# Kernel tuning notes

Measured on AMD Instinct MI355X. Metric: run time of the kernel, lower is better.

## Reference

```python
import jax, jax.numpy as jnp
import numpy as np

NEG_SLOPE = 0.2  # PyG GATConv default LeakyReLU slope
EPS = 1e-16
LN_EPS = 1e-5


def setup_inputs() -> dict:
    key = jax.random.key(0)
    ks = jax.random.split(key, 12)
    N, E, HID, H = 10000, 320000, 256, 4
    C = HID // H
    s = 1.0 / np.sqrt(HID)
    x = jax.random.normal(ks[0], (N, HID), jnp.float32)
    src = jax.random.randint(ks[1], (E,), 0, N, dtype=jnp.int32)
    dst = jax.random.randint(ks[2], (E,), 0, N, dtype=jnp.int32)
    edge_index = jnp.stack([src, dst])
    edge_attr = jax.random.normal(ks[3], (E, 1), jnp.float32)
    W = jax.random.normal(ks[4], (HID, HID), jnp.float32) * s
    att_src = jax.random.normal(ks[5], (H, C), jnp.float32) * s
    att_dst = jax.random.normal(ks[6], (H, C), jnp.float32) * s
    We = jax.random.normal(ks[7], (1, HID), jnp.float32) * s
    att_edge = jax.random.normal(ks[8], (H, C), jnp.float32) * s
    bias = jnp.zeros((HID,), jnp.float32)
    gamma = jnp.ones((HID,), jnp.float32)
    beta = jnp.zeros((HID,), jnp.float32)
    return {"x": x, "edge_index": edge_index, "edge_attr": edge_attr, "W": W,
            "att_src": att_src, "att_dst": att_dst, "We": We,
            "att_edge": att_edge, "bias": bias, "gamma": gamma, "beta": beta}


def _gat_layer(x, edge_index, edge_attr, W, att_src, att_dst, We, att_edge,
               bias, gamma, beta):
    N, HID = x.shape
    H, C = att_src.shape
    src, dst = edge_index[0], edge_index[1]

    # add_self_loops=True with fill_value='mean': self-loop edge_attr is the
    # mean of incoming edge features per node (0 if no incoming edges).
    ones = jnp.ones((src.shape[0],), x.dtype)
    deg = jax.ops.segment_sum(ones, dst, num_segments=N)
    loop_attr = jax.ops.segment_sum(edge_attr, dst, num_segments=N) \
        / jnp.maximum(deg, 1.0)[:, None]
    loop_idx = jnp.arange(N, dtype=src.dtype)
    src = jnp.concatenate([src, loop_idx])
    dst = jnp.concatenate([dst, loop_idx])
    e_attr = jnp.concatenate([edge_attr, loop_attr], axis=0)  # [E+N, 1]

    # node / edge projections
    xp = (x @ W).reshape(N, H, C)                 # [N,H,C]
    a_s = jnp.einsum('nhc,hc->nh', xp, att_src)   # [N,H]
    a_d = jnp.einsum('nhc,hc->nh', xp, att_dst)
    ep = (e_attr @ We).reshape(-1, H, C)          # [E+N,H,C]
    a_e = jnp.einsum('ehc,hc->eh', ep, att_edge)  # [E+N,H]

    logits = a_s[src] + a_d[dst] + a_e            # [E+N,H]
    logits = jax.nn.leaky_relu(logits, NEG_SLOPE)

    # segment softmax over destination neighborhoods
    m = jax.ops.segment_max(logits, dst, num_segments=N)    # [N,H]
    p = jnp.exp(logits - m[dst])
    z = jax.ops.segment_sum(p, dst, num_segments=N)         # [N,H]
    alpha = p / (z[dst] + EPS)                              # [E+N,H]

    # gather-weight-scatter messages
    msg = xp[src] * alpha[:, :, None]                       # [E+N,H,C]
    out = jax.ops.segment_sum(msg, dst, num_segments=N)     # [N,H,C]
    out = out.reshape(N, H * C) + bias

    # LayerNorm (per node over features) + residual + ReLU (dropout in eval)
    mu = jnp.mean(out, axis=-1, keepdims=True)
    var = jnp.var(out, axis=-1, keepdims=True)
    h = (out - mu) * jax.lax.rsqrt(var + LN_EPS) * gamma + beta
    return jax.nn.relu(h + x)


def reference(x, edge_index, edge_attr, W, att_src, att_dst, We, att_edge,
              bias, gamma, beta):
    return _gat_layer(x, edge_index, edge_attr, W, att_src, att_dst, We,
                      att_edge, bias, gamma, beta)
```

## Files before the change

kernel.cpp:

```cpp
#include <hip/hip_runtime.h>

#define HID 256
#define NH 4
#define NEG 0.2f
#define SUBSTRIDE 24
#define NODESTRIDE 192

typedef __attribute__((ext_vector_type(8))) short short8;
typedef __attribute__((ext_vector_type(4))) float f32x4;

__device__ __forceinline__ unsigned short f2b(float f) {
    unsigned u = __float_as_uint(f);
    u = u + 0x7FFFu + ((u >> 16) & 1u);
    return (unsigned short)(u >> 16);
}
__device__ __forceinline__ float b2f_lo(unsigned u) {
    return __uint_as_float(u << 16);
}
__device__ __forceinline__ float b2f_hi(unsigned u) {
    return __uint_as_float(u & 0xFFFF0000u);
}
__device__ __forceinline__ float lrelu(float f) {
    return f > 0.f ? f : NEG * f;
}

__global__ __launch_bounds__(256) void k_init(
    const float* __restrict__ W, const float* __restrict__ We,
    const float* __restrict__ att_edge, unsigned short* __restrict__ Bp,
    float* __restrict__ wedot, int* __restrict__ deg8, int N, int ZB) {
    __shared__ unsigned short sm[4096];
    int b = blockIdx.x, t = threadIdx.x;
    if (b < ZB) {
        int i = b * 256 + t;
        if (i < N * 2) ((int4*)deg8)[i] = make_int4(0, 0, 0, 0);
        return;
    }
    int b2 = b - ZB;
    if (b2 < 16) {
        int n16 = b2;
        int k = t;
        int ks = k >> 5;
        int lhi = ((k & 31) >> 3) << 4;
        int j = k & 7;
        const float4* W4 = (const float4*)W;
        #pragma unroll
        for (int q = 0; q < 4; q++) {
            float4 v = W4[(size_t)k * 64 + n16 * 4 + q];
            int c = q << 2;
            sm[ks * 512 + (lhi + c + 0) * 8 + j] = f2b(v.x);
            sm[ks * 512 + (lhi + c + 1) * 8 + j] = f2b(v.y);
            sm[ks * 512 + (lhi + c + 2) * 8 + j] = f2b(v.z);
            sm[ks * 512 + (lhi + c + 3) * 8 + j] = f2b(v.w);
        }
        __syncthreads();
        uint4* out = (uint4*)(Bp + (size_t)n16 * 4096);
        const uint4* smv = (const uint4*)sm;
        out[t] = smv[t];
        out[256 + t] = smv[256 + t];
    } else {
        float v = We[t] * att_edge[t];
        #pragma unroll
        for (int off = 32; off; off >>= 1) v += __shfl_down(v, off);
        if ((t & 63) == 0) wedot[t >> 6] = v;
    }
}

__global__ __launch_bounds__(256) void k_capmm(
    const int* __restrict__ src, const int* __restrict__ dst,
    const float* __restrict__ eattr, const float* __restrict__ x,
    const unsigned short* __restrict__ Bp, const float* __restrict__ att_src,
    const float* __restrict__ att_dst, unsigned short* __restrict__ xp,
    float* __restrict__ a_s, float* __restrict__ a_d, int* __restrict__ deg8,
    int2* __restrict__ adj, int N, int E, int DBc, int MF) {
    __shared__ unsigned short smA[16384];
    int t = threadIdx.x;
    if ((int)blockIdx.x < DBc) {
        int base = blockIdx.x * 2048 + t;
        #pragma unroll
        for (int q = 0; q < 8; q++) {
            int e = base + q * 256;
            if (e < E) {
                int d = dst[e];
                int sub = e & 7;
                int p = atomicAdd(&deg8[(d << 3) | sub], 1);
                if (p < SUBSTRIDE)
                    adj[(size_t)d * NODESTRIDE + sub * SUBSTRIDE + p] =
                        make_int2(src[e], __float_as_int(eattr[e]));
            }
        }
        return;
    }
    int fi0 = (blockIdx.x - DBc) * 4;
    {
        int r = t >> 4;
        const float4* x4 = (const float4*)x;
        #pragma unroll
        for (int mi = 0; mi < 4; mi++) {
            int row = (fi0 + mi) * 16 + r;
            #pragma unroll
            for (int q = 0; q < 4; q++) {
                int c4 = (t & 15) + (q << 4);
                unsigned u0 = 0, u1 = 0;
                if (row < N) {
                    float4 v = x4[(size_t)row * 64 + c4];
                    u0 = (unsigned)f2b(v.x) | ((unsigned)f2b(v.y) << 16);
                    u1 = (unsigned)f2b(v.z) | ((unsigned)f2b(v.w) << 16);
                }
                int k0 = c4 << 2;
                int ks = k0 >> 5, ko = k0 & 31;
                int lane = r + ((ko >> 3) << 4);
                int off = mi * 4096 + ks * 512 + lane * 8 + (ko & 7);
                *((uint2*)&smA[off]) = make_uint2(u0, u1);
            }
        }
    }
    __syncthreads();
    int w = t >> 6, l = t & 63;
    const short8* B8 = (const short8*)Bp;
    f32x4 acc[4][4];
    #pragma unroll
    for (int mi = 0; mi < 4; mi++)
        #pragma unroll
        for (int ni = 0; ni < 4; ni++)
            acc[mi][ni] = (f32x4){0.f, 0.f, 0.f, 0.f};
    #pragma unroll
    for (int ks = 0; ks < 8; ks++) {
        short8 a[4], b[4];
        #pragma unroll
        for (int mi = 0; mi < 4; mi++)
            a[mi] = *(const short8*)&smA[mi * 4096 + (ks * 64 + l) * 8];
        #pragma unroll
        for (int ni = 0; ni < 4; ni++)
            b[ni] = B8[(size_t)(((w << 2) + ni) * 8 + ks) * 64 + l];
        #pragma unroll
        for (int mi = 0; mi < 4; mi++)
            #pragma unroll
            for (int ni = 0; ni < 4; ni++)
                acc[mi][ni] = __builtin_amdgcn_mfma_f32_16x16x32_bf16(
                    a[mi], b[ni], acc[mi][ni], 0, 0, 0);
    }
    int colb = w << 6;
    float asc[4], adc[4];
    #pragma unroll
    for (int ni = 0; ni < 4; ni++) {
        asc[ni] = att_src[colb + ni * 16 + (l & 15)];
        adc[ni] = att_dst[colb + ni * 16 + (l & 15)];
    }
    #pragma unroll
    for (int mi = 0; mi < 4; mi++) {
        int rowb = fi0 * 16 + mi * 16 + ((l >> 4) << 2);
        #pragma unroll
        for (int r = 0; r < 4; r++) {
            int row = rowb + r;
            float ps = 0.f, pd = 0.f;
            #pragma unroll
            for (int ni = 0; ni < 4; ni++) {
                float v = acc[mi][ni][r];
                ps += v * asc[ni];
                pd += v * adc[ni];
            }
            #pragma unroll
            for (int off = 1; off < 16; off <<= 1) {
                ps += __shfl_xor(ps, off);
                pd += __shfl_xor(pd, off);
            }
            if (row < N) {
                if ((l & 15) == 0) {
                    a_s[(row << 2) + w] = ps;
                    a_d[(row << 2) + w] = pd;
                }
                #pragma unroll
                for (int ni = 0; ni < 4; ni++)
                    xp[(size_t)row * HID + colb + ni * 16 + (l & 15)] =
                        f2b(acc[mi][ni][r]);
            }
        }
    }
}

__global__ __launch_bounds__(256) void k_gather_ln(
    const int2* __restrict__ adj, const int* __restrict__ deg8,
    const float4* __restrict__ a_s4, const float4* __restrict__ a_d4,
    const float* __restrict__ wedot, const unsigned short* __restrict__ xp,
    const float4* __restrict__ x4, const float4* __restrict__ bias4,
    const float4* __restrict__ gamma4, const float4* __restrict__ beta4,
    float4* __restrict__ out4, int N) {
    __shared__ float4 sp[4][64];
    int t = threadIdx.x;
    int u = t >> 6, l = t & 63, hl = l >> 4;
    int n = blockIdx.x * 4 + u;
    if (n >= N) return;
    int vsub = (l < 8) ? deg8[(n << 3) + l] : 0;
    int pre[9];
    pre[0] = 0;
    #pragma unroll
    for (int k = 0; k < 8; k++) pre[k + 1] = pre[k] + __shfl(vsub, k);
    int cnt = pre[8];
    const int2* adjn = adj + (size_t)n * NODESTRIDE;
    float4 adn = a_d4[n];
    float4 wh = *(const float4*)wedot;
    float4 zl = {0.f, 0.f, 0.f, 0.f};
    float sel = 0.f;
    float acc0 = 0.f, acc1 = 0.f, acc2 = 0.f, acc3 = 0.f;
    int ntile = (cnt + 63) >> 6;
    for (int tile = 0; tile < ntile; tile++) {
        int j = (tile << 6) + l;
        float4 p = {0.f, 0.f, 0.f, 0.f};
        float ea = 0.f;
        int s = 0;
        if (j < cnt) {
            int kk = 0, prek = 0;
            #pragma unroll
            for (int q = 1; q < 8; q++) {
                int ge = (j >= pre[q]);
                kk += ge;
                prek = ge ? pre[q] : prek;
            }
            int2 a = adjn[kk * SUBSTRIDE + (j - prek)];
            s = a.x;
            ea = __int_as_float(a.y);
            float4 as_ = a_s4[s];
            p.x = __expf(lrelu(as_.x + adn.x + ea * wh.x));
            p.y = __expf(lrelu(as_.y + adn.y + ea * wh.y));
            p.z = __expf(lrelu(as_.z + adn.z + ea * wh.z));
            p.w = __expf(lrelu(as_.w + adn.w + ea * wh.w));
        }
        zl.x += p.x;
        zl.y += p.y;
        zl.z += p.z;
        zl.w += p.w;
        sel += ea;
        sp[u][l] = p;
        const float* spf = (const float*)&sp[u][0];
        int lim = min(64, cnt - (tile << 6));
        int jj = 0;
        for (; jj + 8 <= lim; jj += 8) {
            int s_[8];
            float p_[8];
            uint2 r_[8];
            #pragma unroll
            for (int k = 0; k < 8; k++)
                s_[k] = __builtin_amdgcn_readfirstlane(__shfl(s, jj + k));
            #pragma unroll
            for (int k = 0; k < 8; k++) {
                p_[k] = spf[(jj + k) * 4 + hl];
                r_[k] = *(const uint2*)(xp + (size_t)s_[k] * HID + 4 * l);
            }
            #pragma unroll
            for (int k = 0; k < 8; k++) {
                acc0 += p_[k] * b2f_lo(r_[k].x);
                acc1 += p_[k] * b2f_hi(r_[k].x);
                acc2 += p_[k] * b2f_lo(r_[k].y);
                acc3 += p_[k] * b2f_hi(r_[k].y);
            }
        }
        for (; jj < lim; jj++) {
            int sj = __builtin_amdgcn_readfirstlane(__shfl(s, jj));
            float pj = spf[jj * 4 + hl];
            uint2 r = *(const uint2*)(xp + (size_t)sj * HID + 4 * l);
            acc0 += pj * b2f_lo(r.x);
            acc1 += pj * b2f_hi(r.x);
            acc2 += pj * b2f_lo(r.y);
            acc3 += pj * b2f_hi(r.y);
        }
    }
    #pragma unroll
    for (int off = 32; off; off >>= 1) {
        zl.x += __shfl_xor(zl.x, off);
        zl.y += __shfl_xor(zl.y, off);
        zl.z += __shfl_xor(zl.z, off);
        zl.w += __shfl_xor(zl.w, off);
        sel += __shfl_xor(sel, off);
    }
    float loop_ea = sel / fmaxf((float)cnt, 1.0f);
    float4 asn = a_s4[n];
    float4 pf;
    pf.x = __expf(lrelu(asn.x + adn.x + loop_ea * wh.x));
    pf.y = __expf(lrelu(asn.y + adn.y + loop_ea * wh.y));
    pf.z = __expf(lrelu(asn.z + adn.z + loop_ea * wh.z));
    pf.w = __expf(lrelu(asn.w + adn.w + loop_ea * wh.w));
    zl.x += pf.x;
    zl.y += pf.y;
    zl.z += pf.z;
    zl.w += pf.w;
    float psl = hl < 2 ? (hl == 0 ? pf.x : pf.y) : (hl == 2 ? pf.z : pf.w);
    uint2 rv = *(const uint2*)(xp + (size_t)n * HID + 4 * l);
    acc0 += psl * b2f_lo(rv.x);
    acc1 += psl * b2f_hi(rv.x);
    acc2 += psl * b2f_lo(rv.y);
    acc3 += psl * b2f_hi(rv.y);
    float zh = hl < 2 ? (hl == 0 ? zl.x : zl.y) : (hl == 2 ? zl.z : zl.w);
    float zi = 1.0f / (zh + 1e-16f);
    float4 bi = bias4[l];
    float v0 = acc0 * zi + bi.x;
    float v1 = acc1 * zi + bi.y;
    float v2 = acc2 * zi + bi.z;
    float v3 = acc3 * zi + bi.w;
    float s1 = v0 + v1 + v2 + v3;
    float s2 = v0 * v0 + v1 * v1 + v2 * v2 + v3 * v3;
    #pragma unroll
    for (int off = 32; off; off >>= 1) {
        s1 += __shfl_xor(s1, off);
        s2 += __shfl_xor(s2, off);
    }
    float mu = s1 * (1.0f / HID);
    float var = s2 * (1.0f / HID) - mu * mu;
    float rstd = rsqrtf(var + 1e-5f);
    float4 g = gamma4[l], be = beta4[l], xr = x4[(size_t)n * 64 + l];
    float4 o;
    o.x = (v0 - mu) * rstd * g.x + be.x + xr.x;
    o.y = (v1 - mu) * rstd * g.y + be.y + xr.y;
    o.z = (v2 - mu) * rstd * g.z + be.z + xr.z;
    o.w = (v3 - mu) * rstd * g.w + be.w + xr.w;
    o.x = o.x > 0.f ? o.x : 0.f;
    o.y = o.y > 0.f ? o.y : 0.f;
    o.z = o.z > 0.f ? o.z : 0.f;
    o.w = o.w > 0.f ? o.w : 0.f;
    out4[(size_t)n * 64 + l] = o;
}

extern "C" void kernel_launch(void* const* d_in, const int* in_sizes, int n_in,
                              void* d_out, int out_size, void* d_ws,
                              size_t ws_size, hipStream_t stream) {
    const float* x        = (const float*)d_in[0];
    const int*   ei       = (const int*)d_in[1];
    const float* eattr    = (const float*)d_in[2];
    const float* W        = (const float*)d_in[3];
    const float* att_src  = (const float*)d_in[4];
    const float* att_dst  = (const float*)d_in[5];
    const float* We       = (const float*)d_in[6];
    const float* att_edge = (const float*)d_in[7];
    const float* bias     = (const float*)d_in[8];
    const float* gamma    = (const float*)d_in[9];
    const float* beta     = (const float*)d_in[10];

    int N = in_sizes[0] / HID;
    int E = in_sizes[1] / 2;
    const int* src = ei;
    const int* dst = ei + E;

    int MF = (N + 15) / 16;
    size_t NP = (size_t)MF * 16;

    float* base = (float*)d_ws;
    unsigned short* Bp = (unsigned short*)base;
    unsigned short* xp = (unsigned short*)(base + 32768);
    float* a_s    = base + 32768 + NP * 128;
    float* a_d    = a_s + (size_t)N * 4;
    float* wedot  = a_d + (size_t)N * 4;
    int* deg8     = (int*)(wedot + 8);
    int2* adj     = (int2*)(deg8 + (size_t)N * 8);

    int ZB = (N * 2 + 255) / 256;
    k_init<<<ZB + 17, 256, 0, stream>>>(W, We, att_edge, Bp, wedot, deg8, N,
                                        ZB);

    int DBc = (E + 2047) / 2048;
    int MB = (MF + 3) / 4;
    k_capmm<<<DBc + MB, 256, 0, stream>>>(src, dst, eattr, x, Bp, att_src,
                                          att_dst, xp, a_s, a_d, deg8, adj, N,
                                          E, DBc, MF);

    k_gather_ln<<<(N + 3) / 4, 256, 0, stream>>>(
        adj, deg8, (const float4*)a_s, (const float4*)a_d, wedot, xp,
        (const float4*)x, (const float4*)bias, (const float4*)gamma,
        (const float4*)beta, (float4*)d_out, N);
}
```

Measured before the change: 54.69 us.

## Split each node's edge list across two wavefronts and combine via shared memory

The gather/LayerNorm kernel now assigns two wavefronts per destination node, each processing half of the incoming edges. Partial accumulators, softmax denominators and edge-attribute sums are exchanged through shared memory after a block barrier, and the first wave finishes the node. This doubles the number of waves in flight to hide gather latency, at the cost of a __syncthreads, extra LDS traffic, twice the blocks, and idle second waves during the LayerNorm tail.

```diff
diff --git a/kernel.cpp b/kernel.cpp
--- a/kernel.cpp
+++ b/kernel.cpp
@@ -186,29 +186,37 @@
     const float4* __restrict__ gamma4, const float4* __restrict__ beta4,
     float4* __restrict__ out4, int N) {
     __shared__ float4 sp[4][64];
+    __shared__ float4 part_acc[4][64];
+    __shared__ float part_z[4][8];
     int t = threadIdx.x;
     int u = t >> 6, l = t & 63, hl = l >> 4;
-    int n = blockIdx.x * 4 + u;
-    if (n >= N) return;
-    int vsub = (l < 8) ? deg8[(n << 3) + l] : 0;
+    int wp = u & 1;
+    int n = blockIdx.x * 2 + (u >> 1);
+    bool active = (n < N);
+    int vsub = (active && l < 8) ? deg8[(n << 3) + l] : 0;
     int pre[9];
     pre[0] = 0;
     #pragma unroll
     for (int k = 0; k < 8; k++) pre[k + 1] = pre[k] + __shfl(vsub, k);
     int cnt = pre[8];
+    int ha = (cnt + 1) >> 1;
+    int wbeg = wp * ha;
+    int wlim = min(cnt, wbeg + ha) - wbeg;
+    if (wlim < 0) wlim = 0;
     const int2* adjn = adj + (size_t)n * NODESTRIDE;
-    float4 adn = a_d4[n];
+    float4 adn = active ? a_d4[n] : (float4){0.f, 0.f, 0.f, 0.f};
     float4 wh = *(const float4*)wedot;
     float4 zl = {0.f, 0.f, 0.f, 0.f};
     float sel = 0.f;
     float acc0 = 0.f, acc1 = 0.f, acc2 = 0.f, acc3 = 0.f;
-    int ntile = (cnt + 63) >> 6;
+    int ntile = (wlim + 63) >> 6;
     for (int tile = 0; tile < ntile; tile++) {
-        int j = (tile << 6) + l;
+        int jl = (tile << 6) + l;
+        int j = wbeg + jl;
         float4 p = {0.f, 0.f, 0.f, 0.f};
         float ea = 0.f;
         int s = 0;
-        if (j < cnt) {
+        if (jl < wlim) {
             int kk = 0, prek = 0;
             #pragma unroll
             for (int q = 1; q < 8; q++) {
@@ -232,7 +240,7 @@
         sel += ea;
         sp[u][l] = p;
         const float* spf = (const float*)&sp[u][0];
-        int lim = min(64, cnt - (tile << 6));
+        int lim = min(64, wlim - (tile << 6));
         int jj = 0;
         for (; jj + 8 <= lim; jj += 8) {
             int s_[8];
@@ -271,6 +279,28 @@
         zl.z += __shfl_xor(zl.z, off);
         zl.w += __shfl_xor(zl.w, off);
         sel += __shfl_xor(sel, off);
+    }
+    part_acc[u][l] = make_float4(acc0, acc1, acc2, acc3);
+    if (l == 0) {
+        part_z[u][0] = zl.x;
+        part_z[u][1] = zl.y;
+        part_z[u][2] = zl.z;
+        part_z[u][3] = zl.w;
+        part_z[u][4] = sel;
+    }
+    __syncthreads();
+    if (wp != 0 || !active) return;
+    {
+        float4 pa = part_acc[u + 1][l];
+        acc0 += pa.x;
+        acc1 += pa.y;
+        acc2 += pa.z;
+        acc3 += pa.w;
+        zl.x += part_z[u + 1][0];
+        zl.y += part_z[u + 1][1];
+        zl.z += part_z[u + 1][2];
+        zl.w += part_z[u + 1][3];
+        sel += part_z[u + 1][4];
     }
     float loop_ea = sel / fmaxf((float)cnt, 1.0f);
     float4 asn = a_s4[n];
@@ -361,7 +391,7 @@
                                           att_dst, xp, a_s, a_d, deg8, adj, N,
                                           E, DBc, MF);
 
-    k_gather_ln<<<(N + 3) / 4, 256, 0, stream>>>(
+    k_gather_ln<<<(N + 1) / 2, 256, 0, stream>>>(
         adj, deg8, (const float4*)a_s, (const float4*)a_d, wedot, xp,
         (const float4*)x, (const float4*)bias, (const float4*)gamma,
         (const float4*)beta, (float4*)d_out, N);
```

After: 60.36 us. 10.4% more time.
